# Kernel tuning notes

Hardware: AMD Instinct MI355X
Metric: run time of the kernel (lower is better)

## Reference

```python
import jax, jax.numpy as jnp
import numpy as np
from jax import lax

B, P, ENC, H, A, E, V, TC = 64, 196, 2048, 1024, 1024, 512, 10000, 32


def setup_inputs() -> dict:
    key = jax.random.key(0)
    ks = jax.random.split(key, 24)
    s = 0.02
    inp = {
        'enc_out': jax.random.normal(ks[0], (B, P, ENC), jnp.float32),
        'enc_captions': jax.random.randint(ks[1], (B, TC), 0, V),
        'lengths': jax.random.randint(ks[2], (B,), 2, TC + 1).at[0].set(TC),
        'W_enc_att': jax.random.normal(ks[3], (A, ENC)) * s,
        'b_enc_att': jnp.zeros((A,)),
        'W_dec_att': jax.random.normal(ks[4], (A, H)) * s,
        'b_dec_att': jnp.zeros((A,)),
        'W_full': jax.random.normal(ks[5], (1, A)) * s,
        'b_full': jnp.zeros((1,)),
        'emb': jax.random.uniform(ks[6], (V, E), minval=-0.1, maxval=0.1),
        'W_ih': jax.random.normal(ks[7], (4 * H, E + ENC)) * s,
        'b_ih': jnp.zeros((4 * H,)),
        'W_hh': jax.random.normal(ks[8], (4 * H, H)) * s,
        'b_hh': jnp.zeros((4 * H,)),
        'W_init_h': jax.random.normal(ks[9], (H, ENC)) * s,
        'b_init_h': jnp.zeros((H,)),
        'W_init_c': jax.random.normal(ks[10], (H, ENC)) * s,
        'b_init_c': jnp.zeros((H,)),
        'W_beta': jax.random.normal(ks[11], (ENC, H)) * s,
        'b_beta': jnp.zeros((ENC,)),
        'W_fc': jax.random.uniform(ks[12], (V, H), minval=-0.1, maxval=0.1),
        'b_fc': jnp.zeros((V,)),
    }
    return inp


def reference(enc_out, enc_captions, lengths,
              W_enc_att, b_enc_att, W_dec_att, b_dec_att, W_full, b_full,
              emb, W_ih, b_ih, W_hh, b_hh,
              W_init_h, b_init_h, W_init_c, b_init_c,
              W_beta, b_beta, W_fc, b_fc):
    T = enc_captions.shape[1] - 1  # static max decode length (setup forces one full-length row)
    ind = jnp.argsort(-lengths)
    lens = lengths[ind]
    eo = enc_out[ind]              # [B,P,ENC] sorted by length desc
    caps = enc_captions[ind]
    dec_lens = lens - 1
    embs = emb[caps]               # [B,TC,E]

    mean_a = eo.mean(axis=1)
    h0 = mean_a @ W_init_h.T + b_init_h
    c0 = mean_a @ W_init_c.T + b_init_c

    # encoder projection is time-invariant; hoist out of the loop
    enc_att = jnp.einsum('bpe,ae->bpa', eo, W_enc_att) + b_enc_att  # [B,P,A]

    mask_ts = jnp.arange(T)[:, None] < dec_lens[None, :]            # [T,B]
    emb_ts = jnp.swapaxes(embs[:, :T, :], 0, 1)                     # [T,B,E]

    def step(carry, xs):
        h, c = carry
        emb_t, m = xs  # [B,E], [B] bool (active rows = leading batch_size_t)
        # attention
        dec = h @ W_dec_att.T + b_dec_att                            # [B,A]
        a = jax.nn.relu(enc_att + dec[:, None, :]) @ W_full[0] + b_full[0]  # [B,P]
        alpha = jax.nn.softmax(a, axis=1)
        context = jnp.einsum('bpe,bp->be', eo, alpha)                # [B,ENC]
        # gate + LSTM cell (torch gate order: i, f, g, o)
        gate = jax.nn.sigmoid(h @ W_beta.T + b_beta)
        awe = gate * context
        x = jnp.concatenate([emb_t, awe], axis=1)
        gates = x @ W_ih.T + b_ih + h @ W_hh.T + b_hh
        i, f, g, o = jnp.split(gates, 4, axis=1)
        c_new = jax.nn.sigmoid(f) * c + jax.nn.sigmoid(i) * jnp.tanh(g)
        h_new = jax.nn.sigmoid(o) * jnp.tanh(c_new)
        m2 = m[:, None]
        h2 = jnp.where(m2, h_new, h)  # inactive rows keep frozen state
        c2 = jnp.where(m2, c_new, c)
        mf = m2.astype(h.dtype)
        preds = (h_new @ W_fc.T + b_fc) * mf  # dropout = identity (eval)
        return (h2, c2), (preds, alpha * mf)

    (_, _), (preds, alphas) = lax.scan(step, (h0, c0), (emb_ts, mask_ts))
    predictions = jnp.swapaxes(preds, 0, 1)   # [B,T,V]
    alphas = jnp.swapaxes(alphas, 0, 1)       # [B,T,P]
    return predictions, alphas, caps, dec_lens, ind
```

## Files before the change

kernel.cpp:

```cpp
#include <hip/hip_runtime.h>

#define Bn   64
#define Pp   196
#define ENCd 2048
#define Hd   1024
#define Ad   1024
#define Ed   512
#define Vd   10000
#define TCd  32
#define Td   31
#define XHW  3584
#define VPAD 10240
#define KHL  6144

typedef short bf16x8 __attribute__((ext_vector_type(8)));
typedef float f32x4  __attribute__((ext_vector_type(4)));

static __device__ __forceinline__ float bf2f(unsigned short u) {
    unsigned int x = ((unsigned int)u) << 16;
    float f; __builtin_memcpy(&f, &x, 4); return f;
}
static __device__ __forceinline__ unsigned short f2bf(float f) {
    unsigned int x; __builtin_memcpy(&x, &f, 4);
    x += 0x7fffu + ((x >> 16) & 1u);
    return (unsigned short)(x >> 16);
}
static __device__ __forceinline__ float sigf(float x) { return 1.f / (1.f + expf(-x)); }

static __device__ __forceinline__ void gl_lds16(const unsigned short* g, unsigned short* l) {
    __builtin_amdgcn_global_load_lds((const __attribute__((address_space(1))) void*)g,
                                     (__attribute__((address_space(3))) void*)l,
                                     16, 0, 0);
}


__global__ void sort_kernel(const int* __restrict__ lengths, const int* __restrict__ captions,
                            int* __restrict__ ind, int* __restrict__ dl,
                            float* __restrict__ out_caps, float* __restrict__ out_dl,
                            float* __restrict__ out_ind) {
    __shared__ int s_ind[Bn];
    int tid = threadIdx.x;
    int Lt = lengths[tid];
    int pos = 0;
    for (int k = 0; k < Bn; ++k) {
        int Lk = lengths[k];
        pos += (Lk > Lt) || (Lk == Lt && k < tid);
    }
    s_ind[pos] = tid;
    __syncthreads();
    int src = s_ind[tid];
    ind[tid] = src;
    int d = lengths[src] - 1;
    dl[tid] = d;
    out_ind[tid] = (float)src;
    out_dl[tid] = (float)d;
    for (int j = 0; j < TCd; ++j)
        out_caps[tid * TCd + j] = (float)captions[src * TCd + j];
}

__global__ void cvt_kernel(const float* __restrict__ src, unsigned short* __restrict__ dst, int n) {
    int i = blockIdx.x * 256 + threadIdx.x;
    int stride = gridDim.x * 256;
    for (; i < n; i += stride) dst[i] = f2bf(src[i]);
}

__global__ void wcat_kernel(const float* __restrict__ wih, const float* __restrict__ whh,
                            unsigned short* __restrict__ wcat) {
    int j = blockIdx.y;
    int idx = blockIdx.x * 256 + threadIdx.x;
    float v = (idx < 2560) ? wih[(size_t)j * 2560 + idx] : whh[(size_t)j * 1024 + (idx - 2560)];
    wcat[(size_t)j * XHW + idx] = f2bf(v);
}

__global__ void biascat_kernel(const float* __restrict__ bih, const float* __restrict__ bhh,
                               float* __restrict__ bc) {
    int i = blockIdx.x * 256 + threadIdx.x;
    bc[i] = bih[i] + bhh[i];
}

__global__ void gather_eo_kernel(const float* __restrict__ enc_out, const int* __restrict__ ind,
                                 unsigned short* __restrict__ eo) {
    int b = blockIdx.y;
    int idx = blockIdx.x * 256 + threadIdx.x;
    int src = ind[b];
    eo[(size_t)b * (Pp * ENCd) + idx] = f2bf(enc_out[(size_t)src * (Pp * ENCd) + idx]);
}

__global__ void mean_kernel(const float* __restrict__ enc_out, const int* __restrict__ ind,
                            float* __restrict__ meanf) {
    int b = blockIdx.y;
    int e = blockIdx.x * 256 + threadIdx.x;
    int src = ind[b];
    const float* base = enc_out + (size_t)src * (Pp * ENCd) + e;
    float s = 0.f;
    for (int p = 0; p < Pp; ++p) s += base[(size_t)p * ENCd];
    meanf[b * ENCd + e] = s * (1.f / 196.f);
}

__global__ void embs_kernel(const float* __restrict__ emb, const int* __restrict__ captions,
                            const int* __restrict__ ind, unsigned short* __restrict__ xhbuf) {
    int b = blockIdx.y;
    int idx = blockIdx.x * 256 + threadIdx.x;
    int t = idx >> 9, e = idx & 511;
    int src = ind[b];
    int cap = captions[src * TCd + t];
    xhbuf[((size_t)t * Bn + b) * XHW + e] = f2bf(emb[(size_t)cap * Ed + e]);
}

__global__ void hilo_w_kernel(const float* __restrict__ winh, const float* __restrict__ winc,
                              unsigned short* __restrict__ dst) {
    int n = blockIdx.y;
    int k = blockIdx.x * 256 + threadIdx.x;
    const float* src = (n < 1024) ? (winh + (size_t)n * ENCd)
                                  : (winc + (size_t)(n - 1024) * ENCd);
    float v = src[k];
    unsigned short hi = f2bf(v);
    unsigned short lo = f2bf(v - bf2f(hi));
    size_t row = (size_t)n * KHL;
    dst[row + k]        = hi;
    dst[row + 2048 + k] = hi;
    dst[row + 4096 + k] = lo;
}

__global__ void hilo_a_kernel(const float* __restrict__ meanf, unsigned short* __restrict__ dst) {
    int id = blockIdx.x * 256 + threadIdx.x;
    int m = id >> 11, k = id & 2047;
    float v = meanf[id];
    unsigned short hi = f2bf(v);
    unsigned short lo = f2bf(v - bf2f(hi));
    size_t row = (size_t)m * KHL;
    dst[row + k]        = hi;
    dst[row + 2048 + k] = lo;
    dst[row + 4096 + k] = hi;
}

__global__ void initred_kernel(const float* __restrict__ part,
                               const float* __restrict__ binh, const float* __restrict__ binc,
                               unsigned short* __restrict__ xh0, float* __restrict__ cbuf) {
    int id = blockIdx.x * 256 + threadIdx.x;
    int m = id >> 11, n = id & 2047;
    bool is_c = n >= 1024;
    int nn = is_c ? n - 1024 : n;
    float acc = is_c ? binc[nn] : binh[nn];
#pragma unroll
    for (int s = 0; s < 8; ++s)
        acc += part[((size_t)(s * Bn + m)) * 2048 + n];
    if (is_c) cbuf[(size_t)m * Hd + nn] = acc;
    else      xh0[(size_t)m * XHW + 2560 + nn] = f2bf(acc);
}

template<int EPI, int SWZ>
__global__ __launch_bounds__(256)
void gemm_tile(const unsigned short* __restrict__ A, int lda,
               const unsigned short* __restrict__ W, int ldw,
               const float* __restrict__ bias,
               int N, int nbn, int K,
               float* __restrict__ outf, unsigned short* __restrict__ outb, int ldo,
               const int* __restrict__ dl) {
    __shared__ unsigned short lA[128 * 32];
    __shared__ unsigned short lB[128 * 32];

    int tid  = threadIdx.x;
    int wave = tid >> 6, lane = tid & 63;
    int bid = blockIdx.x;
    if (SWZ) {
        int cpx = gridDim.x >> 3;
        bid = (bid & 7) * cpx + (bid >> 3);
    }
    int mt = bid / nbn;
    int nt = bid % nbn;
    int m0 = mt * 128, n0 = nt * 128;

    int rs = lane >> 2;
    int cs = (lane & 3) * 8;
    const unsigned short* aG0 = A + (size_t)(m0 + wave * 16 + rs) * lda + cs;
    const unsigned short* aG1 = aG0 + (size_t)64 * lda;
    const unsigned short* bG0 = W + (size_t)(n0 + wave * 16 + rs) * ldw + cs;
    const unsigned short* bG1 = bG0 + (size_t)64 * ldw;
    unsigned short* lA0 = &lA[(wave * 16) * 32];
    unsigned short* lA1 = &lA[(64 + wave * 16) * 32];
    unsigned short* lB0 = &lB[(wave * 16) * 32];
    unsigned short* lB1 = &lB[(64 + wave * 16) * 32];

    int wr = wave >> 1, wc = wave & 1;
    int col = lane & 15, quad = lane >> 4;

    f32x4 acc[4][4];
#pragma unroll
    for (int i = 0; i < 4; ++i)
#pragma unroll
        for (int j = 0; j < 4; ++j) acc[i][j] = (f32x4){0.f, 0.f, 0.f, 0.f};

    for (int kt = 0; kt < K; kt += 32) {
        __syncthreads();
        gl_lds16(aG0 + kt, lA0);
        gl_lds16(aG1 + kt, lA1);
        gl_lds16(bG0 + kt, lB0);
        gl_lds16(bG1 + kt, lB1);
        __syncthreads();

        bf16x8 af[4], bf[4];
#pragma unroll
        for (int i = 0; i < 4; ++i) {
            af[i] = *(const bf16x8*)&lA[(wr * 64 + i * 16 + col) * 32 + quad * 8];
            bf[i] = *(const bf16x8*)&lB[(wc * 64 + i * 16 + col) * 32 + quad * 8];
        }
#pragma unroll
        for (int mi = 0; mi < 4; ++mi)
#pragma unroll
            for (int nj = 0; nj < 4; ++nj)
                acc[mi][nj] = __builtin_amdgcn_mfma_f32_16x16x32_bf16(af[mi], bf[nj], acc[mi][nj], 0, 0, 0);
    }

#pragma unroll
    for (int mi = 0; mi < 4; ++mi) {
#pragma unroll
        for (int r = 0; r < 4; ++r) {
            int m = m0 + wr * 64 + mi * 16 + quad * 4 + r;
            if (EPI == 5 && m >= Td * Bn) continue;
#pragma unroll
            for (int nj = 0; nj < 4; ++nj) {
                int n = n0 + wc * 64 + nj * 16 + col;
                if (EPI == 1) {
                    outb[(size_t)m * ldo + n] = f2bf(acc[mi][nj][r] + bias[n]);
                } else {
                    if (n < N) {
                        int t = m >> 6, b = m & 63;
                        float mf = (t < dl[b]) ? 1.f : 0.f;
                        float v = acc[mi][nj][r] + bias[n];
                        outf[((size_t)b * Td + t) * Vd + n] = v * mf;
                    }
                }
            }
        }
    }
}

template<int SK>
__global__ void gemm_sk4(const unsigned short* __restrict__ A, int lda,
                         const unsigned short* __restrict__ W,
                         int N, int K, float* __restrict__ part) {
    int wid  = (blockIdx.x * 256 + threadIdx.x) >> 6;
    int lane = threadIdx.x & 63;
    int ntiles = N >> 4;
    int s = wid / ntiles;
    int nt = wid - s * ntiles;
    int col = lane & 15, quad = lane >> 4;
    int kLen = K / SK, k0 = s * kLen;

    const unsigned short* aptr = A + (size_t)col * lda + k0 + quad * 8;
    const unsigned short* wptr = W + (size_t)(nt * 16 + col) * K + k0 + quad * 8;

    f32x4 acc[4];
#pragma unroll
    for (int i = 0; i < 4; ++i) acc[i] = (f32x4){0.f, 0.f, 0.f, 0.f};

    for (int k = 0; k < kLen; k += 32) {
        bf16x8 wf = *(const bf16x8*)(wptr + k);
#pragma unroll
        for (int mi = 0; mi < 4; ++mi) {
            bf16x8 af = *(const bf16x8*)(aptr + (size_t)mi * 16 * lda + k);
            acc[mi] = __builtin_amdgcn_mfma_f32_16x16x32_bf16(af, wf, acc[mi], 0, 0, 0);
        }
    }

    int n = nt * 16 + col;
    float* base = part + (size_t)s * Bn * N;
#pragma unroll
    for (int mi = 0; mi < 4; ++mi) {
#pragma unroll
        for (int r = 0; r < 4; ++r) {
            int m = mi * 16 + quad * 4 + r;
            base[(size_t)m * N + n] = acc[mi][r];
        }
    }
}


__global__ void scores_kernel(const float* __restrict__ pdb, const float* __restrict__ bdec,
                              const unsigned short* __restrict__ encatt,
                              const float* __restrict__ wfull,
                              float* __restrict__ scores) {
    int b = blockIdx.y;
    int tid = threadIdx.x;
    __shared__ float sdec[Ad];
    for (int i = tid; i < Ad; i += 256) {
        float v = bdec[i];
#pragma unroll
        for (int s2 = 0; s2 < 4; ++s2) v += pdb[((size_t)(s2 * Bn + b)) * 3072 + i];
        sdec[i] = v;
    }
    __syncthreads();
    int wave = tid >> 6, lane = tid & 63;
    int p = blockIdx.x * 4 + wave;
    const unsigned int* ea = (const unsigned int*)(encatt + ((size_t)(b * Pp + p) << 10));
    const float2* dp = (const float2*)sdec;
    const float2* wf = (const float2*)wfull;
    float acc = 0.f;
#pragma unroll
    for (int it = 0; it < 8; ++it) {
        int i2 = it * 64 + lane;
        unsigned int u = ea[i2];
        float2 dv = dp[i2];
        float2 wv = wf[i2];
        acc += fmaxf(bf2f((unsigned short)(u & 0xffffu)) + dv.x, 0.f) * wv.x;
        acc += fmaxf(bf2f((unsigned short)(u >> 16)) + dv.y, 0.f) * wv.y;
    }
    for (int o2 = 32; o2; o2 >>= 1) acc += __shfl_xor(acc, o2);
    if (lane == 0) scores[b * Pp + p] = acc;
}

__global__ void softmaxctx_kernel(const float* __restrict__ scores,
                                  const float* __restrict__ pdb, const float* __restrict__ bbeta,
                                  const unsigned short* __restrict__ eo,
                                  unsigned short* __restrict__ xh_t,
                                  float* __restrict__ out_alpha,
                                  const int* __restrict__ dl, int t) {
    int b = blockIdx.y, tid = threadIdx.x;
    __shared__ float red[256];
    __shared__ float sal[Pp];
    float s = (tid < Pp) ? scores[b * Pp + tid] : -1e30f;
    red[tid] = s; __syncthreads();
    for (int o2 = 128; o2; o2 >>= 1) { if (tid < o2) red[tid] = fmaxf(red[tid], red[tid + o2]); __syncthreads(); }
    float mx = red[0]; __syncthreads();
    float e = (tid < Pp) ? expf(s - mx) : 0.f;
    red[tid] = e; __syncthreads();
    for (int o2 = 128; o2; o2 >>= 1) { if (tid < o2) red[tid] += red[tid + o2]; __syncthreads(); }
    float inv = 1.f / red[0];
    if (tid < Pp) {
        float a = e * inv;
        sal[tid] = a;
        if (blockIdx.x == 0) {
            float mf = (t < dl[b]) ? 1.f : 0.f;
            out_alpha[((size_t)b * Td + t) * Pp + tid] = a * mf;
        }
    }
    __syncthreads();

    int e0 = blockIdx.x * 512 + tid * 2;
    const unsigned int* base = (const unsigned int*)(eo + (size_t)b * Pp * ENCd);
    int half = e0 >> 1;
    float a0 = 0.f, a1 = 0.f;
    for (int p = 0; p < Pp; ++p) {
        unsigned int u = base[p * (ENCd / 2) + half];
        float w = sal[p];
        a0 += w * bf2f((unsigned short)(u & 0xffffu));
        a1 += w * bf2f((unsigned short)(u >> 16));
    }
    float g0 = bbeta[e0], g1 = bbeta[e0 + 1];
#pragma unroll
    for (int s2 = 0; s2 < 4; ++s2) {
        const float* pb = pdb + ((size_t)(s2 * Bn + b)) * 3072 + Ad + e0;
        g0 += pb[0]; g1 += pb[1];
    }
    g0 = sigf(g0); g1 = sigf(g1);
    xh_t[(size_t)b * XHW + 512 + e0]     = f2bf(a0 * g0);
    xh_t[(size_t)b * XHW + 512 + e0 + 1] = f2bf(a1 * g1);
}

__global__ void lstm_kernel(const float* __restrict__ pg, const float* __restrict__ biascat,
                            float* __restrict__ c,
                            const unsigned short* __restrict__ xh_cur,
                            unsigned short* __restrict__ xh_next,
                            unsigned short* __restrict__ hall, const int* __restrict__ dl, int t) {
    int id = blockIdx.x * 256 + threadIdx.x;
    int b = id >> 10, j = id & 1023;
    float iv = biascat[j], fv = biascat[1024 + j], gv = biascat[2048 + j], ov = biascat[3072 + j];
#pragma unroll
    for (int s2 = 0; s2 < 8; ++s2) {
        const float* base = pg + ((size_t)(s2 * Bn + b)) * 4096;
        iv += base[j]; fv += base[1024 + j]; gv += base[2048 + j]; ov += base[3072 + j];
    }
    float co = c[id];
    float cn = sigf(fv) * co + sigf(iv) * tanhf(gv);
    float hn = sigf(ov) * tanhf(cn);
    bool m = t < dl[b];
    float ho = bf2f(xh_cur[(size_t)b * XHW + 2560 + j]);
    float h2 = m ? hn : ho;
    c[id] = m ? cn : co;
    xh_next[(size_t)b * XHW + 2560 + j] = f2bf(h2);
    hall[((size_t)t * Bn + b) * Hd + j] = f2bf(hn);
}


extern "C" void kernel_launch(void* const* d_in, const int* in_sizes, int n_in,
                              void* d_out, int out_size, void* d_ws, size_t ws_size,
                              hipStream_t stream) {
    const float* enc_out   = (const float*)d_in[0];
    const int*   captions  = (const int*)d_in[1];
    const int*   lengths   = (const int*)d_in[2];
    const float* W_enc_att = (const float*)d_in[3];
    const float* b_enc_att = (const float*)d_in[4];
    const float* W_dec_att = (const float*)d_in[5];
    const float* b_dec_att = (const float*)d_in[6];
    const float* W_full    = (const float*)d_in[7];
    const float* emb       = (const float*)d_in[9];
    const float* W_ih      = (const float*)d_in[10];
    const float* b_ih      = (const float*)d_in[11];
    const float* W_hh      = (const float*)d_in[12];
    const float* b_hh      = (const float*)d_in[13];
    const float* W_init_h  = (const float*)d_in[14];
    const float* b_init_h  = (const float*)d_in[15];
    const float* W_init_c  = (const float*)d_in[16];
    const float* b_init_c  = (const float*)d_in[17];
    const float* W_beta    = (const float*)d_in[18];
    const float* b_beta    = (const float*)d_in[19];
    const float* W_fc      = (const float*)d_in[20];
    const float* b_fc      = (const float*)d_in[21];

    float* out       = (float*)d_out;
    float* out_pred  = out;
    float* out_alpha = out + (size_t)Bn * Td * Vd;
    float* out_caps  = out_alpha + (size_t)Bn * Td * Pp;
    float* out_dl    = out_caps + (size_t)Bn * TCd;
    float* out_ind   = out_dl + Bn;

    char* ws = (char*)d_ws;
    size_t off = 0;
    auto take = [&](size_t n) -> char* {
        char* p = ws + off;
        off = (off + n + 255) & ~(size_t)255;
        return p;
    };
    int* ind_i   = (int*)take(Bn * 4);
    int* dl_i    = (int*)take(Bn * 4);
    unsigned short* eo_b     = (unsigned short*)take((size_t)Bn * Pp * ENCd * 2);
    unsigned short* encatt_b = (unsigned short*)take((size_t)Bn * Pp * Ad * 2);
    unsigned short* wcat_b   = (unsigned short*)take((size_t)4096 * XHW * 2);
    unsigned short* wfc_b    = (unsigned short*)take((size_t)VPAD * Hd * 2);
    unsigned short* wenc_b   = (unsigned short*)take((size_t)Ad * ENCd * 2);
    unsigned short* wdb_b    = (unsigned short*)take((size_t)3072 * Hd * 2);
    float*          biascat  = (float*)take(4096 * 4);
    float*          meanf    = (float*)take((size_t)Bn * ENCd * 4);
    unsigned short* xhbuf    = (unsigned short*)take((size_t)32 * Bn * XHW * 2);
    float*          cbuf     = (float*)take((size_t)Bn * Hd * 4);
    unsigned short* hall     = (unsigned short*)take((size_t)2048 * Hd * 2);
    float*          scores   = (float*)take((size_t)Bn * Pp * 4);
    float*          pdb      = (float*)take((size_t)4 * Bn * 3072 * 4);
    float*          pgates   = (float*)take((size_t)8 * Bn * 4096 * 4);
    unsigned short* ahl      = (unsigned short*)take((size_t)Bn * KHL * 2);
    unsigned short* whl   = encatt_b;
    float*          pinit = pgates;
    (void)ws_size; (void)out_size; (void)n_in; (void)in_sizes;

    sort_kernel<<<1, 64, 0, stream>>>(lengths, captions, ind_i, dl_i, out_caps, out_dl, out_ind);

    auto cvt = [&](const float* s, unsigned short* d, int n) {
        int g = (n + 255) / 256; if (g > 4096) g = 4096;
        cvt_kernel<<<g, 256, 0, stream>>>(s, d, n);
    };
    cvt(W_enc_att, wenc_b, Ad * ENCd);
    cvt(W_dec_att, wdb_b, Ad * Hd);
    cvt(W_beta,  wdb_b + (size_t)Ad * Hd, ENCd * Hd);
    cvt(W_fc,    wfc_b,   Vd * Hd);
    wcat_kernel<<<dim3(14, 4096), 256, 0, stream>>>(W_ih, W_hh, wcat_b);
    biascat_kernel<<<16, 256, 0, stream>>>(b_ih, b_hh, biascat);

    gather_eo_kernel<<<dim3(1568, Bn), 256, 0, stream>>>(enc_out, ind_i, eo_b);
    mean_kernel<<<dim3(8, Bn), 256, 0, stream>>>(enc_out, ind_i, meanf);
    embs_kernel<<<dim3(62, Bn), 256, 0, stream>>>(emb, captions, ind_i, xhbuf);

    hilo_w_kernel<<<dim3(8, 2048), 256, 0, stream>>>(W_init_h, W_init_c, whl);
    hilo_a_kernel<<<512, 256, 0, stream>>>(meanf, ahl);
    gemm_sk4<8><<<256, 256, 0, stream>>>(ahl, KHL, whl, 2048, KHL, pinit);
    initred_kernel<<<512, 256, 0, stream>>>(pinit, b_init_h, b_init_c, xhbuf, cbuf);

    gemm_tile<1, 1><<<98 * 8, 256, 0, stream>>>(eo_b, ENCd, wenc_b, ENCd, b_enc_att,
        Ad, 8, ENCd, nullptr, encatt_b, Ad, nullptr);

    for (int t = 0; t < Td; ++t) {
        unsigned short* xh_t = xhbuf + (size_t)t * Bn * XHW;
        unsigned short* xh_n = xhbuf + (size_t)(t + 1) * Bn * XHW;

        gemm_sk4<4><<<192, 256, 0, stream>>>(xh_t + 2560, XHW, wdb_b, 3072, Hd, pdb);

        scores_kernel<<<dim3(49, Bn), 256, 0, stream>>>(pdb, b_dec_att, encatt_b, W_full, scores);

        softmaxctx_kernel<<<dim3(4, Bn), 256, 0, stream>>>(scores, pdb, b_beta, eo_b,
            xh_t, out_alpha, dl_i, t);

        gemm_sk4<8><<<512, 256, 0, stream>>>(xh_t, XHW, wcat_b, 4096, XHW, pgates);

        lstm_kernel<<<256, 256, 0, stream>>>(pgates, biascat, cbuf, xh_t, xh_n, hall, dl_i, t);
    }

    gemm_tile<5, 0><<<16 * 80, 256, 0, stream>>>(hall, Hd, wfc_b, Hd, b_fc,
        Vd, 80, Hd, out_pred, nullptr, 0, dl_i);
}
```

Measured before the change: 2.315 ms.

## Fuse LSTM gate GEMM with cell update using interleaved gate weights

Reorders the concatenated W_ih/W_hh rows and the summed biases so the four gates of each hidden unit sit next to each other. This lets a single MFMA kernel compute a 32-column gate slice and apply the LSTM cell update in its epilogue. It replaces the split-K gate GEMM, its fp32 partial-sum buffer and the separate LSTM kernel with one launch per timestep. The cost is only 128 blocks with a two-way K split reduced through shared memory, so there is less parallelism and no LDS staging of the activations.

Measured after the change: 2.669 ms. 15.3% more time.

```diff
diff --git a/kernel.cpp b/kernel.cpp
--- a/kernel.cpp
+++ b/kernel.cpp
@@ -66,16 +66,18 @@
 
 __global__ void wcat_kernel(const float* __restrict__ wih, const float* __restrict__ whh,
                             unsigned short* __restrict__ wcat) {
-    int j = blockIdx.y;
+    int r = blockIdx.y;
     int idx = blockIdx.x * 256 + threadIdx.x;
-    float v = (idx < 2560) ? wih[(size_t)j * 2560 + idx] : whh[(size_t)j * 1024 + (idx - 2560)];
-    wcat[(size_t)j * XHW + idx] = f2bf(v);
+    int js = (r & 3) * 1024 + (r >> 2);
+    float v = (idx < 2560) ? wih[(size_t)js * 2560 + idx] : whh[(size_t)js * 1024 + (idx - 2560)];
+    wcat[(size_t)r * XHW + idx] = f2bf(v);
 }
 
 __global__ void biascat_kernel(const float* __restrict__ bih, const float* __restrict__ bhh,
                                float* __restrict__ bc) {
-    int i = blockIdx.x * 256 + threadIdx.x;
-    bc[i] = bih[i] + bhh[i];
+    int r = blockIdx.x * 256 + threadIdx.x;
+    int js = (r & 3) * 1024 + (r >> 2);
+    bc[r] = bih[js] + bhh[js];
 }
 
 __global__ void gather_eo_kernel(const float* __restrict__ enc_out, const int* __restrict__ ind,
@@ -358,28 +360,65 @@
     xh_t[(size_t)b * XHW + 512 + e0 + 1] = f2bf(a1 * g1);
 }
 
-__global__ void lstm_kernel(const float* __restrict__ pg, const float* __restrict__ biascat,
-                            float* __restrict__ c,
-                            const unsigned short* __restrict__ xh_cur,
-                            unsigned short* __restrict__ xh_next,
-                            unsigned short* __restrict__ hall, const int* __restrict__ dl, int t) {
-    int id = blockIdx.x * 256 + threadIdx.x;
-    int b = id >> 10, j = id & 1023;
-    float iv = biascat[j], fv = biascat[1024 + j], gv = biascat[2048 + j], ov = biascat[3072 + j];
-#pragma unroll
-    for (int s2 = 0; s2 < 8; ++s2) {
-        const float* base = pg + ((size_t)(s2 * Bn + b)) * 4096;
-        iv += base[j]; fv += base[1024 + j]; gv += base[2048 + j]; ov += base[3072 + j];
-    }
-    float co = c[id];
-    float cn = sigf(fv) * co + sigf(iv) * tanhf(gv);
-    float hn = sigf(ov) * tanhf(cn);
-    bool m = t < dl[b];
-    float ho = bf2f(xh_cur[(size_t)b * XHW + 2560 + j]);
-    float h2 = m ? hn : ho;
-    c[id] = m ? cn : co;
-    xh_next[(size_t)b * XHW + 2560 + j] = f2bf(h2);
-    hall[((size_t)t * Bn + b) * Hd + j] = f2bf(hn);
+__global__ __launch_bounds__(256)
+void gates_lstm_kernel(const unsigned short* __restrict__ xh_cur,
+                       const unsigned short* __restrict__ wg,
+                       const float* __restrict__ bg,
+                       float* __restrict__ c,
+                       unsigned short* __restrict__ xh_next,
+                       unsigned short* __restrict__ hall,
+                       const int* __restrict__ dl, int t) {
+    __shared__ float lacc[4][64][16];
+    int tid = threadIdx.x;
+    int wave = tid >> 6, lane = tid & 63;
+    int col = lane & 15, quad = lane >> 4;
+    int ntb = wave & 1, kh = wave >> 1;
+    int n0 = blockIdx.x * 32 + ntb * 16;
+    int k0 = kh * (XHW / 2);
+
+    const unsigned short* aptr = xh_cur + (size_t)col * XHW + k0 + quad * 8;
+    const unsigned short* wptr = wg + (size_t)(n0 + col) * XHW + k0 + quad * 8;
+
+    f32x4 acc[4];
+#pragma unroll
+    for (int i = 0; i < 4; ++i) acc[i] = (f32x4){0.f, 0.f, 0.f, 0.f};
+
+    for (int k = 0; k < XHW / 2; k += 32) {
+        bf16x8 wf = *(const bf16x8*)(wptr + k);
+#pragma unroll
+        for (int mi = 0; mi < 4; ++mi) {
+            bf16x8 af = *(const bf16x8*)(aptr + (size_t)mi * 16 * XHW + k);
+            acc[mi] = __builtin_amdgcn_mfma_f32_16x16x32_bf16(af, wf, acc[mi], 0, 0, 0);
+        }
+    }
+#pragma unroll
+    for (int mi = 0; mi < 4; ++mi)
+#pragma unroll
+        for (int r = 0; r < 4; ++r)
+            lacc[wave][mi * 16 + quad * 4 + r][col] = acc[mi][r];
+    __syncthreads();
+
+#pragma unroll
+    for (int it = 0; it < 2; ++it) {
+        int pid = tid + it * 256;
+        int b = pid >> 3;
+        int ub = pid & 7;
+        int w0 = ub >> 2;
+        int cb = (ub & 3) * 4;
+        int j = blockIdx.x * 8 + ub;
+        float i_ = bg[4 * j + 0] + (lacc[w0][b][cb + 0] + lacc[w0 + 2][b][cb + 0]);
+        float f_ = bg[4 * j + 1] + (lacc[w0][b][cb + 1] + lacc[w0 + 2][b][cb + 1]);
+        float g_ = bg[4 * j + 2] + (lacc[w0][b][cb + 2] + lacc[w0 + 2][b][cb + 2]);
+        float o_ = bg[4 * j + 3] + (lacc[w0][b][cb + 3] + lacc[w0 + 2][b][cb + 3]);
+        float co = c[b * Hd + j];
+        float cn = sigf(f_) * co + sigf(i_) * tanhf(g_);
+        float hn = sigf(o_) * tanhf(cn);
+        bool m = t < dl[b];
+        float ho = bf2f(xh_cur[(size_t)b * XHW + 2560 + j]);
+        c[b * Hd + j] = m ? cn : co;
+        xh_next[(size_t)b * XHW + 2560 + j] = f2bf(m ? hn : ho);
+        hall[((size_t)t * Bn + b) * Hd + j] = f2bf(hn);
+    }
 }
 
 
@@ -437,10 +476,9 @@
     unsigned short* hall     = (unsigned short*)take((size_t)2048 * Hd * 2);
     float*          scores   = (float*)take((size_t)Bn * Pp * 4);
     float*          pdb      = (float*)take((size_t)4 * Bn * 3072 * 4);
-    float*          pgates   = (float*)take((size_t)8 * Bn * 4096 * 4);
+    float*          pinit    = (float*)take((size_t)8 * Bn * 2048 * 4);
     unsigned short* ahl      = (unsigned short*)take((size_t)Bn * KHL * 2);
     unsigned short* whl   = encatt_b;
-    float*          pinit = pgates;
     (void)ws_size; (void)out_size; (void)n_in; (void)in_sizes;
 
     sort_kernel<<<1, 64, 0, stream>>>(lengths, captions, ind_i, dl_i, out_caps, out_dl, out_ind);
@@ -479,9 +517,8 @@
         softmaxctx_kernel<<<dim3(4, Bn), 256, 0, stream>>>(scores, pdb, b_beta, eo_b,
             xh_t, out_alpha, dl_i, t);
 
-        gemm_sk4<8><<<512, 256, 0, stream>>>(xh_t, XHW, wcat_b, 4096, XHW, pgates);
-
-        lstm_kernel<<<256, 256, 0, stream>>>(pgates, biascat, cbuf, xh_t, xh_n, hall, dl_i, t);
+        gates_lstm_kernel<<<128, 256, 0, stream>>>(xh_t, wcat_b, biascat, cbuf,
+            xh_n, hall, dl_i, t);
     }
 
     gemm_tile<5, 0><<<16 * 80, 256, 0, stream>>>(hall, Hd, wfc_b, Hd, b_fc,
```

## Skip finished sequences in per-step decode kernels using active-row counts

Applied to the files above, without the earlier changes.

Computes per-timestep active batch counts in the sort kernel and uses them to skip inactive rows. The attention scores, softmax-context and LSTM kernels return early for those rows, and the split-K GEMMs skip 16-row MFMA tiles that are entirely inactive. Alpha output is pre-zeroed once so skipped rows stay zero, and inactive rows copy their hidden state forward. This relies on rows being sorted by length so that active rows form a prefix. The savings are limited by the 16-row granularity and by the weight loads, which are still issued.

New measurement: 2.098 ms. 9.4% less time.

```diff
diff --git a/kernel.cpp b/kernel.cpp
--- a/kernel.cpp
+++ b/kernel.cpp
@@ -37,8 +37,9 @@
 __global__ void sort_kernel(const int* __restrict__ lengths, const int* __restrict__ captions,
                             int* __restrict__ ind, int* __restrict__ dl,
                             float* __restrict__ out_caps, float* __restrict__ out_dl,
-                            float* __restrict__ out_ind) {
+                            float* __restrict__ out_ind, int* __restrict__ nact) {
     __shared__ int s_ind[Bn];
+    __shared__ int s_dl[Bn];
     int tid = threadIdx.x;
     int Lt = lengths[tid];
     int pos = 0;
@@ -52,10 +53,22 @@
     ind[tid] = src;
     int d = lengths[src] - 1;
     dl[tid] = d;
+    s_dl[tid] = d;
     out_ind[tid] = (float)src;
     out_dl[tid] = (float)d;
     for (int j = 0; j < TCd; ++j)
         out_caps[tid * TCd + j] = (float)captions[src * TCd + j];
+    __syncthreads();
+    if (tid < Td) {
+        int cnt = 0;
+        for (int b = 0; b < Bn; ++b) cnt += (s_dl[b] > tid) ? 1 : 0;
+        nact[tid] = cnt;
+    }
+}
+
+__global__ void zero_alpha_kernel(float* __restrict__ a, int n) {
+    int i = blockIdx.x * 256 + threadIdx.x;
+    if (i < n) a[i] = 0.f;
 }
 
 __global__ void cvt_kernel(const float* __restrict__ src, unsigned short* __restrict__ dst, int n) {
@@ -226,9 +239,8 @@
                 } else {
                     if (n < N) {
                         int t = m >> 6, b = m & 63;
-                        float mf = (t < dl[b]) ? 1.f : 0.f;
                         float v = acc[mi][nj][r] + bias[n];
-                        outf[((size_t)b * Td + t) * Vd + n] = v * mf;
+                        outf[((size_t)b * Td + t) * Vd + n] = (t < dl[b]) ? v : 0.f;
                     }
                 }
             }
@@ -239,7 +251,10 @@
 template<int SK>
 __global__ void gemm_sk4(const unsigned short* __restrict__ A, int lda,
                          const unsigned short* __restrict__ W,
-                         int N, int K, float* __restrict__ part) {
+                         int N, int K, float* __restrict__ part,
+                         const int* __restrict__ nact, int t) {
+    int mtn = 4;
+    if (nact) mtn = (nact[t] + 15) >> 4;
     int wid  = (blockIdx.x * 256 + threadIdx.x) >> 6;
     int lane = threadIdx.x & 63;
     int ntiles = N >> 4;
@@ -259,8 +274,10 @@
         bf16x8 wf = *(const bf16x8*)(wptr + k);
 #pragma unroll
         for (int mi = 0; mi < 4; ++mi) {
-            bf16x8 af = *(const bf16x8*)(aptr + (size_t)mi * 16 * lda + k);
-            acc[mi] = __builtin_amdgcn_mfma_f32_16x16x32_bf16(af, wf, acc[mi], 0, 0, 0);
+            if (mi < mtn) {
+                bf16x8 af = *(const bf16x8*)(aptr + (size_t)mi * 16 * lda + k);
+                acc[mi] = __builtin_amdgcn_mfma_f32_16x16x32_bf16(af, wf, acc[mi], 0, 0, 0);
+            }
         }
     }
 
@@ -268,10 +285,12 @@
     float* base = part + (size_t)s * Bn * N;
 #pragma unroll
     for (int mi = 0; mi < 4; ++mi) {
-#pragma unroll
-        for (int r = 0; r < 4; ++r) {
-            int m = mi * 16 + quad * 4 + r;
-            base[(size_t)m * N + n] = acc[mi][r];
+        if (mi < mtn) {
+#pragma unroll
+            for (int r = 0; r < 4; ++r) {
+                int m = mi * 16 + quad * 4 + r;
+                base[(size_t)m * N + n] = acc[mi][r];
+            }
         }
     }
 }
@@ -280,8 +299,10 @@
 __global__ void scores_kernel(const float* __restrict__ pdb, const float* __restrict__ bdec,
                               const unsigned short* __restrict__ encatt,
                               const float* __restrict__ wfull,
-                              float* __restrict__ scores) {
+                              float* __restrict__ scores,
+                              const int* __restrict__ nact, int t) {
     int b = blockIdx.y;
+    if (b >= nact[t]) return;
     int tid = threadIdx.x;
     __shared__ float sdec[Ad];
     for (int i = tid; i < Ad; i += 256) {
@@ -315,8 +336,10 @@
                                   const unsigned short* __restrict__ eo,
                                   unsigned short* __restrict__ xh_t,
                                   float* __restrict__ out_alpha,
-                                  const int* __restrict__ dl, int t) {
-    int b = blockIdx.y, tid = threadIdx.x;
+                                  const int* __restrict__ nact, int t) {
+    int b = blockIdx.y;
+    if (b >= nact[t]) return;
+    int tid = threadIdx.x;
     __shared__ float red[256];
     __shared__ float sal[Pp];
     float s = (tid < Pp) ? scores[b * Pp + tid] : -1e30f;
@@ -331,8 +354,7 @@
         float a = e * inv;
         sal[tid] = a;
         if (blockIdx.x == 0) {
-            float mf = (t < dl[b]) ? 1.f : 0.f;
-            out_alpha[((size_t)b * Td + t) * Pp + tid] = a * mf;
+            out_alpha[((size_t)b * Td + t) * Pp + tid] = a;
         }
     }
     __syncthreads();
@@ -362,9 +384,14 @@
                             float* __restrict__ c,
                             const unsigned short* __restrict__ xh_cur,
                             unsigned short* __restrict__ xh_next,
-                            unsigned short* __restrict__ hall, const int* __restrict__ dl, int t) {
+                            unsigned short* __restrict__ hall,
+                            const int* __restrict__ nact, int t) {
     int id = blockIdx.x * 256 + threadIdx.x;
     int b = id >> 10, j = id & 1023;
+    if (b >= nact[t]) {
+        xh_next[(size_t)b * XHW + 2560 + j] = xh_cur[(size_t)b * XHW + 2560 + j];
+        return;
+    }
     float iv = biascat[j], fv = biascat[1024 + j], gv = biascat[2048 + j], ov = biascat[3072 + j];
 #pragma unroll
     for (int s2 = 0; s2 < 8; ++s2) {
@@ -374,12 +401,10 @@
     float co = c[id];
     float cn = sigf(fv) * co + sigf(iv) * tanhf(gv);
     float hn = sigf(ov) * tanhf(cn);
-    bool m = t < dl[b];
-    float ho = bf2f(xh_cur[(size_t)b * XHW + 2560 + j]);
-    float h2 = m ? hn : ho;
-    c[id] = m ? cn : co;
-    xh_next[(size_t)b * XHW + 2560 + j] = f2bf(h2);
-    hall[((size_t)t * Bn + b) * Hd + j] = f2bf(hn);
+    unsigned short hb = f2bf(hn);
+    c[id] = cn;
+    xh_next[(size_t)b * XHW + 2560 + j] = hb;
+    hall[((size_t)t * Bn + b) * Hd + j] = hb;
 }
 
 
@@ -424,6 +449,7 @@
     };
     int* ind_i   = (int*)take(Bn * 4);
     int* dl_i    = (int*)take(Bn * 4);
+    int* nact_d  = (int*)take(Td * 4);
     unsigned short* eo_b     = (unsigned short*)take((size_t)Bn * Pp * ENCd * 2);
     unsigned short* encatt_b = (unsigned short*)take((size_t)Bn * Pp * Ad * 2);
     unsigned short* wcat_b   = (unsigned short*)take((size_t)4096 * XHW * 2);
@@ -443,7 +469,9 @@
     float*          pinit = pgates;
     (void)ws_size; (void)out_size; (void)n_in; (void)in_sizes;
 
-    sort_kernel<<<1, 64, 0, stream>>>(lengths, captions, ind_i, dl_i, out_caps, out_dl, out_ind);
+    sort_kernel<<<1, 64, 0, stream>>>(lengths, captions, ind_i, dl_i, out_caps, out_dl,
+                                      out_ind, nact_d);
+    zero_alpha_kernel<<<(Bn * Td * Pp + 255) / 256, 256, 0, stream>>>(out_alpha, Bn * Td * Pp);
 
     auto cvt = [&](const float* s, unsigned short* d, int n) {
         int g = (n + 255) / 256; if (g > 4096) g = 4096;
@@ -462,7 +490,7 @@
 
     hilo_w_kernel<<<dim3(8, 2048), 256, 0, stream>>>(W_init_h, W_init_c, whl);
     hilo_a_kernel<<<512, 256, 0, stream>>>(meanf, ahl);
-    gemm_sk4<8><<<256, 256, 0, stream>>>(ahl, KHL, whl, 2048, KHL, pinit);
+    gemm_sk4<8><<<256, 256, 0, stream>>>(ahl, KHL, whl, 2048, KHL, pinit, nullptr, 0);
     initred_kernel<<<512, 256, 0, stream>>>(pinit, b_init_h, b_init_c, xhbuf, cbuf);
 
     gemm_tile<1, 1><<<98 * 8, 256, 0, stream>>>(eo_b, ENCd, wenc_b, ENCd, b_enc_att,
@@ -472,16 +500,20 @@
         unsigned short* xh_t = xhbuf + (size_t)t * Bn * XHW;
         unsigned short* xh_n = xhbuf + (size_t)(t + 1) * Bn * XHW;
 
-        gemm_sk4<4><<<192, 256, 0, stream>>>(xh_t + 2560, XHW, wdb_b, 3072, Hd, pdb);
-
-        scores_kernel<<<dim3(49, Bn), 256, 0, stream>>>(pdb, b_dec_att, encatt_b, W_full, scores);
+        gemm_sk4<4><<<192, 256, 0, stream>>>(xh_t + 2560, XHW, wdb_b, 3072, Hd, pdb,
+                                             nact_d, t);
+
+        scores_kernel<<<dim3(49, Bn), 256, 0, stream>>>(pdb, b_dec_att, encatt_b, W_full,
+                                                        scores, nact_d, t);
 
         softmaxctx_kernel<<<dim3(4, Bn), 256, 0, stream>>>(scores, pdb, b_beta, eo_b,
-            xh_t, out_alpha, dl_i, t);
-
-        gemm_sk4<8><<<512, 256, 0, stream>>>(xh_t, XHW, wcat_b, 4096, XHW, pgates);
-
-        lstm_kernel<<<256, 256, 0, stream>>>(pgates, biascat, cbuf, xh_t, xh_n, hall, dl_i, t);
+            xh_t, out_alpha, nact_d, t);
+
+        gemm_sk4<8><<<512, 256, 0, stream>>>(xh_t, XHW, wcat_b, 4096, XHW, pgates,
+                                             nact_d, t);
+
+        lstm_kernel<<<256, 256, 0, stream>>>(pgates, biascat, cbuf, xh_t, xh_n, hall,
+                                             nact_d, t);
     }
 
     gemm_tile<5, 0><<<16 * 80, 256, 0, stream>>>(hall, Hd, wfc_b, Hd, b_fc,
```
